# Optimization experiments

Measured on AMD Instinct MI355X. Metric: run time of the kernel, lower is better.

Reference implementation:

```python
import jax, jax.numpy as jnp
import numpy as np

TEMP = 0.07
W00 = 0.1
EPS = 1e-8


def setup_inputs() -> dict:
    key = jax.random.key(0)
    k1, k2, k3, k4 = jax.random.split(key, 4)
    B, N, D = 32, 256, 256
    M = B * N
    return {
        "audio_feats": jax.random.normal(k1, (B, N, D), dtype=jnp.float32),
        "visual_feats": jax.random.normal(k2, (B, N, D), dtype=jnp.float32),
        "audio_labels": jax.random.randint(k3, (M,), 0, 2, dtype=jnp.int64)
            if jax.config.jax_enable_x64 else jax.random.randint(k3, (M,), 0, 2, dtype=jnp.int32),
        "visual_labels": jax.random.randint(k4, (M,), 0, 2, dtype=jnp.int64)
            if jax.config.jax_enable_x64 else jax.random.randint(k4, (M,), 0, 2, dtype=jnp.int32),
    }


def reference(audio_feats, visual_feats, audio_labels, visual_labels):
    B, N, D = audio_feats.shape
    M = B * N
    a = audio_feats.reshape(M, D)
    v = visual_feats.reshape(M, D)
    # L2 normalize (torch F.normalize uses eps=1e-12 clamp on norm)
    a = a / jnp.maximum(jnp.linalg.norm(a, axis=-1, keepdims=True), 1e-12)
    v = v / jnp.maximum(jnp.linalg.norm(v, axis=-1, keepdims=True), 1e-12)
    sim = (a @ v.T) / TEMP  # (M, M)
    exp_sim = jnp.exp(sim)
    la = audio_labels[:, None]  # (M, 1)
    lv = visual_labels[None, :]  # (1, M)
    pos_mask = (la == lv) & ((la == 1) | (la == 0))
    weight = jnp.where(la == 1, 1.0, W00) * pos_mask.astype(sim.dtype)  # (M, M)
    wexp = exp_sim * weight

    # audio -> visual (row direction)
    denom_a2v = exp_sim.sum(axis=1)
    num_a2v = wexp.sum(axis=1)
    frac_a2v = (num_a2v + EPS) / (denom_a2v + EPS)
    valid_a2v = (num_a2v > 0).astype(sim.dtype)
    loss_a2v = -(valid_a2v * jnp.log(frac_a2v)).sum() / jnp.maximum(valid_a2v.sum(), 1.0)

    # visual -> audio (column direction)
    denom_v2a = exp_sim.sum(axis=0)
    num_v2a = wexp.sum(axis=0)
    frac_v2a = (num_v2a + EPS) / (denom_v2a + EPS)
    valid_v2a = (num_v2a > 0).astype(sim.dtype)
    loss_v2a = -(valid_v2a * jnp.log(frac_v2a)).sum() / jnp.maximum(valid_v2a.sum(), 1.0)

    return 0.5 * (loss_a2v + loss_v2a)
```

## Files before the change

### kernel.cpp

```cpp
#include <hip/hip_runtime.h>

#define M_ROWS 8192
#define D_DIM  256
#define BM     128
#define BN     128
#define NBI    (M_ROWS / BM)
#define NBJ    (M_ROWS / BN)
#define NJOBS  (NBI * NBJ)

#define ALPHA  4.53982478f


typedef __attribute__((ext_vector_type(4))) float  floatx4;

__device__ inline unsigned short f2bf(float f) {
    union { float f; unsigned int u; } v; v.f = f;
    unsigned int u = v.u;
    u = (u + 0x7fffu + ((u >> 16) & 1u)) >> 16;
    return (unsigned short)u;
}

__device__ inline float bf2f(unsigned short b) {
    union { unsigned int u; float f; } v; v.u = (unsigned int)b << 16;
    return v.f;
}

__device__ inline float fast_exp2(float x) {
#if __has_builtin(__builtin_amdgcn_exp2f)
    return __builtin_amdgcn_exp2f(x);
#else
    return exp2f(x);
#endif
}

__global__ __launch_bounds__(256) void normalize_kernel(
    const float* __restrict__ af, const float* __restrict__ vf,
    unsigned char* __restrict__ aB, unsigned char* __restrict__ vB,
    float* __restrict__ glob)
{
    __shared__ unsigned short tileS[16 * 264];

    if (blockIdx.x == 0) {
        if (threadIdx.x < 4) glob[threadIdx.x] = 0.f;
        if (threadIdx.x == 4) ((int*)glob)[4] = 0;
    }

    const int b = blockIdx.x;
    const bool isA = b < 512;
    const int T = isA ? b : b - 512;
    const float* src = (isA ? af : vf) + (size_t)T * 16 * D_DIM;
    unsigned char* dst = (isA ? aB : vB) + (size_t)T * 4096;

    const int t = threadIdx.x;
    const int row = t >> 4, c = t & 15;

    const float* p = src + row * D_DIM + c * 16;
    float4 x0 = ((const float4*)p)[0], x1 = ((const float4*)p)[1];
    float4 x2 = ((const float4*)p)[2], x3 = ((const float4*)p)[3];
    float ss = x0.x*x0.x + x0.y*x0.y + x0.z*x0.z + x0.w*x0.w
             + x1.x*x1.x + x1.y*x1.y + x1.z*x1.z + x1.w*x1.w
             + x2.x*x2.x + x2.y*x2.y + x2.z*x2.z + x2.w*x2.w
             + x3.x*x3.x + x3.y*x3.y + x3.z*x3.z + x3.w*x3.w;
    #pragma unroll
    for (int m = 1; m < 16; m <<= 1) ss += __shfl_xor(ss, m, 64);
    float scale = ALPHA / fmaxf(sqrtf(ss), 1e-12f);

    unsigned short* q = tileS + row * 264 + c * 16;
    ushort4 o0, o1, o2, o3;
    o0.x = f2bf(x0.x*scale); o0.y = f2bf(x0.y*scale); o0.z = f2bf(x0.z*scale); o0.w = f2bf(x0.w*scale);
    o1.x = f2bf(x1.x*scale); o1.y = f2bf(x1.y*scale); o1.z = f2bf(x1.z*scale); o1.w = f2bf(x1.w*scale);
    o2.x = f2bf(x2.x*scale); o2.y = f2bf(x2.y*scale); o2.z = f2bf(x2.z*scale); o2.w = f2bf(x2.w*scale);
    o3.x = f2bf(x3.x*scale); o3.y = f2bf(x3.y*scale); o3.z = f2bf(x3.z*scale); o3.w = f2bf(x3.w*scale);
    ((ushort4*)q)[0] = o0; ((ushort4*)q)[1] = o1;
    ((ushort4*)q)[2] = o2; ((ushort4*)q)[3] = o3;
    __syncthreads();

    #pragma unroll
    for (int s = 0; s < 2; ++s) {
        const int ch  = t + s * 256;
        const int l16 = ch & 15, quad = (ch >> 4) & 3, k32 = ch >> 6;
        const unsigned short* rp = &tileS[l16 * 264 + k32 * 32 + quad * 8];
        float f0 = bf2f(rp[0]), f1 = bf2f(rp[1]), f2 = bf2f(rp[2]), f3 = bf2f(rp[3]);
        float f4 = bf2f(rp[4]), f5 = bf2f(rp[5]), f6 = bf2f(rp[6]), f7 = bf2f(rp[7]);
        int p0 = __builtin_amdgcn_cvt_pk_fp8_f32(f0, f1, 0, false);
        p0     = __builtin_amdgcn_cvt_pk_fp8_f32(f2, f3, p0, true);
        int p1 = __builtin_amdgcn_cvt_pk_fp8_f32(f4, f5, 0, false);
        p1     = __builtin_amdgcn_cvt_pk_fp8_f32(f6, f7, p1, true);
        int2 outv; outv.x = p0; outv.y = p1;
        *(int2*)(dst + (size_t)ch * 8) = outv;
    }
}

__global__ __launch_bounds__(256, 3) void gemm_loss_kernel(
    const unsigned char* __restrict__ aB, const unsigned char* __restrict__ vB,
    const int* __restrict__ la, const int* __restrict__ lv,
    float* __restrict__ rowPart, float* __restrict__ colPart)
{
    const int tid  = threadIdx.x;
    const int wave = tid >> 6, lane = tid & 63;
    const int quad = lane >> 4, l16 = lane & 15;

    const int super = blockIdx.x >> 8;
    const int inner = blockIdx.x & 255;
    const int bx = (super & 3) * 16 + (inner & 15);
    const int by = (super >> 2) * 16 + (inner >> 4);
    const int i0 = bx * BM, j0 = by * BN;

    const unsigned char* Abase = aB + ((size_t)(bx * 8 + wave * 2) * 512 + lane) * 8;
    const unsigned char* Vbase = vB + ((size_t)(by * 8) * 512 + lane) * 8;

    floatx4 acc[2][8] = {};
    long long afr[3][2], bfr[3][8];

    #pragma unroll
    for (int s = 0; s < 2; ++s) {
        #pragma unroll
        for (int it = 0; it < 2; ++it)
            afr[s][it] = *(const long long*)(Abase + it * 4096 + s * 512);
        #pragma unroll
        for (int jt = 0; jt < 8; ++jt)
            bfr[s][jt] = *(const long long*)(Vbase + jt * 4096 + s * 512);
    }

    #pragma unroll
    for (int k32 = 0; k32 < 8; ++k32) {
        const int cur = k32 % 3;
        if (k32 < 6) {
            const int nx = (k32 + 2) % 3;
            const size_t ko = (size_t)(k32 + 2) * 512;
            #pragma unroll
            for (int it = 0; it < 2; ++it)
                afr[nx][it] = *(const long long*)(Abase + it * 4096 + ko);
            #pragma unroll
            for (int jt = 0; jt < 8; ++jt)
                bfr[nx][jt] = *(const long long*)(Vbase + jt * 4096 + ko);
        }
        #pragma unroll
        for (int it = 0; it < 2; ++it)
            #pragma unroll
            for (int jt = 0; jt < 8; ++jt)
                acc[it][jt] = __builtin_amdgcn_mfma_f32_16x16x32_fp8_fp8(
                    afr[cur][it], bfr[cur][jt], acc[it][jt], 0, 0, 0);
    }

    const int baseRow = i0 + wave * 32;
    float maf[2][4];
    #pragma unroll
    for (int it = 0; it < 2; ++it)
        #pragma unroll
        for (int r = 0; r < 4; ++r)
            maf[it][r] = (float)la[baseRow + it * 16 + quad * 4 + r];
    float mvf[8];
    #pragma unroll
    for (int jt = 0; jt < 8; ++jt)
        mvf[jt] = (float)lv[j0 + jt * 16 + l16];

    float rT[2][4] = {}, r1[2][4] = {};
    float cT[8] = {}, c1[8] = {};
    #pragma unroll
    for (int it = 0; it < 2; ++it) {
        #pragma unroll
        for (int jt = 0; jt < 8; ++jt) {
            #pragma unroll
            for (int r = 0; r < 4; ++r) {
                float e = fast_exp2(acc[it][jt][r]);
                rT[it][r] += e;
                r1[it][r] = fmaf(mvf[jt], e, r1[it][r]);
                cT[jt] += e;
                c1[jt] = fmaf(maf[it][r], e, c1[jt]);
            }
        }
    }

    #pragma unroll
    for (int jt = 0; jt < 8; ++jt) {
        float t0 = cT[jt], t1 = c1[jt];
        t0 += __shfl_xor(t0, 16, 64); t0 += __shfl_xor(t0, 32, 64);
        t1 += __shfl_xor(t1, 16, 64); t1 += __shfl_xor(t1, 32, 64);
        cT[jt] = t0; c1[jt] = t1;
    }

    __shared__ float rowbuf[2 * BM];
    __shared__ float colbuf[8 * BN];

    #pragma unroll
    for (int it = 0; it < 2; ++it) {
        #pragma unroll
        for (int r = 0; r < 4; ++r) {
            float s0 = rT[it][r], s1 = r1[it][r];
            #pragma unroll
            for (int m = 1; m < 16; m <<= 1) {
                s0 += __shfl_xor(s0, m, 64);
                s1 += __shfl_xor(s1, m, 64);
            }
            if (l16 == 0) {
                int rl = wave * 32 + it * 16 + quad * 4 + r;
                rowbuf[rl * 2 + 0] = s0;
                rowbuf[rl * 2 + 1] = s1;
            }
        }
    }
    if (quad == 0) {
        #pragma unroll
        for (int jt = 0; jt < 8; ++jt) {
            colbuf[(wave * 2 + 0) * BN + jt * 16 + l16] = cT[jt];
            colbuf[(wave * 2 + 1) * BN + jt * 16 + l16] = c1[jt];
        }
    }
    __syncthreads();

    {
        const int rl  = tid >> 1;
        const int cls = tid & 1;
        rowPart[((size_t)by * M_ROWS + i0 + rl) * 2 + cls] = rowbuf[rl * 2 + cls];
        float s = colbuf[(0 * 2 + cls) * BN + rl] + colbuf[(1 * 2 + cls) * BN + rl]
                + colbuf[(2 * 2 + cls) * BN + rl] + colbuf[(3 * 2 + cls) * BN + rl];
        colPart[((size_t)bx * M_ROWS + j0 + rl) * 2 + cls] = s;
    }
}

__global__ __launch_bounds__(256) void reduce_kernel(
    const float* __restrict__ rowPart, const float* __restrict__ colPart,
    const int* __restrict__ la, const int* __restrict__ lv,
    float* __restrict__ glob, float* __restrict__ out)
{
    const int bid = blockIdx.x;
    const bool aside = bid < 32;
    const int idx = (aside ? bid : bid - 32) * 256 + threadIdx.x;
    const float* part = aside ? rowPart : colPart;
    const int* lab = aside ? la : lv;

    float tot = 0.f, c1 = 0.f;
    #pragma unroll 4
    for (int b = 0; b < 64; ++b) {
        float2 p = *(const float2*)(part + ((size_t)b * M_ROWS + idx) * 2);
        tot += p.x; c1 += p.y;
    }
    float num = lab[idx] ? c1 : 0.1f * (tot - c1);
    float lg = 0.f, cnt = 0.f;
    if (num > 0.f) { lg = logf((num + 1e-8f) / (tot + 1e-8f)); cnt = 1.f; }

    #pragma unroll
    for (int m = 1; m < 64; m <<= 1) {
        lg  += __shfl_xor(lg,  m, 64);
        cnt += __shfl_xor(cnt, m, 64);
    }
    __shared__ float red[4][2];
    const int w = threadIdx.x >> 6, ln = threadIdx.x & 63;
    if (ln == 0) { red[w][0] = lg; red[w][1] = cnt; }
    __syncthreads();
    if (threadIdx.x == 0) {
        float slg  = red[0][0] + red[1][0] + red[2][0] + red[3][0];
        float scnt = red[0][1] + red[1][1] + red[2][1] + red[3][1];
        float* base = glob + (aside ? 0 : 2);
        atomicAdd(&base[0], slg);
        atomicAdd(&base[1], scnt);
        __threadfence();
        int old = atomicAdd((int*)glob + 4, 1);
        if (old == 63) {
            __threadfence();
            float sA = atomicAdd(&glob[0], 0.f);
            float cA = atomicAdd(&glob[1], 0.f);
            float sV = atomicAdd(&glob[2], 0.f);
            float cV = atomicAdd(&glob[3], 0.f);
            float lossA = -sA / fmaxf(cA, 1.f);
            float lossV = -sV / fmaxf(cV, 1.f);
            out[0] = 0.5f * (lossA + lossV);
        }
    }
}

extern "C" void kernel_launch(void* const* d_in, const int* in_sizes, int n_in,
                              void* d_out, int out_size, void* d_ws, size_t ws_size,
                              hipStream_t stream)
{
    const float* af = (const float*)d_in[0];
    const float* vf = (const float*)d_in[1];
    const int*   la = (const int*)d_in[2];
    const int*   lv = (const int*)d_in[3];
    float* out = (float*)d_out;

    char* ws = (char*)d_ws;
    unsigned char* aB = (unsigned char*)ws;
    unsigned char* vB = (unsigned char*)(ws + 2ull * 1024 * 1024);
    float* rowPart   = (float*)(ws +  4ull * 1024 * 1024);
    float* colPart   = (float*)(ws +  8ull * 1024 * 1024);
    float* glob      = (float*)(ws + 12ull * 1024 * 1024);

    normalize_kernel<<<1024, 256, 0, stream>>>(af, vf, aB, vB, glob);
    gemm_loss_kernel<<<NJOBS, 256, 0, stream>>>(aB, vB, la, lv, rowPart, colPart);
    reduce_kernel<<<64, 256, 0, stream>>>(rowPart, colPart, la, lv, glob, out);
}
```

Baseline: 131.0 us.

## Switch to 16x16x128 scaled FP8 MFMA with LDS-staged V tile and direct FP8 quantization

Replaces the 16x16x32 FP8 MFMA with the gfx950 scaled 16x16x128 f8f6f4 MFMA (unit scales), cutting the MFMA instruction count by four. The fp8 layout written by the normalize kernel is changed to match the wider operand fragments. Normalization now reduces the sum of squares through shared memory and quantizes straight to FP8, skipping the bf16 staging tile. In the GEMM kernel the whole 128x256 V tile is staged once in 32KB of LDS, and A fragments are loaded with 16-byte vector loads. The extra LDS footprint may reduce occupancy below the three blocks per CU the kernel requests.

```diff
diff --git a/kernel.cpp b/kernel.cpp
--- a/kernel.cpp
+++ b/kernel.cpp
@@ -11,19 +11,8 @@
 #define ALPHA  4.53982478f
 
 
-typedef __attribute__((ext_vector_type(4))) float  floatx4;
-
-__device__ inline unsigned short f2bf(float f) {
-    union { float f; unsigned int u; } v; v.f = f;
-    unsigned int u = v.u;
-    u = (u + 0x7fffu + ((u >> 16) & 1u)) >> 16;
-    return (unsigned short)u;
-}
-
-__device__ inline float bf2f(unsigned short b) {
-    union { unsigned int u; float f; } v; v.u = (unsigned int)b << 16;
-    return v.f;
-}
+typedef __attribute__((ext_vector_type(4))) float floatx4;
+typedef __attribute__((ext_vector_type(8))) int   intx8;
 
 __device__ inline float fast_exp2(float x) {
 #if __has_builtin(__builtin_amdgcn_exp2f)
@@ -33,12 +22,17 @@
 #endif
 }
 
+__device__ inline floatx4 mfma_fp8(intx8 a, intx8 b, floatx4 c) {
+    return __builtin_amdgcn_mfma_scale_f32_16x16x128_f8f6f4(
+        a, b, c, 0, 0, 0, 0x7f7f7f7f, 0, 0x7f7f7f7f);
+}
+
 __global__ __launch_bounds__(256) void normalize_kernel(
     const float* __restrict__ af, const float* __restrict__ vf,
     unsigned char* __restrict__ aB, unsigned char* __restrict__ vB,
     float* __restrict__ glob)
 {
-    __shared__ unsigned short tileS[16 * 264];
+    __shared__ float ssb[16][4];
 
     if (blockIdx.x == 0) {
         if (threadIdx.x < 4) glob[threadIdx.x] = 0.f;
@@ -51,44 +45,44 @@
     const float* src = (isA ? af : vf) + (size_t)T * 16 * D_DIM;
     unsigned char* dst = (isA ? aB : vB) + (size_t)T * 4096;
 
-    const int t = threadIdx.x;
-    const int row = t >> 4, c = t & 15;
-
-    const float* p = src + row * D_DIM + c * 16;
+    const int t    = threadIdx.x;
+    const int wave = t >> 6, lane = t & 63;
+    const int row  = t & 15;
+    const int kq   = (t >> 4) & 3;
+    const int h    = (t >> 6) & 1;
+    const int s    = t >> 7;
+    const int kbase = s * 128 + kq * 32 + h * 16;
+
+    const float* p = src + row * D_DIM + kbase;
     float4 x0 = ((const float4*)p)[0], x1 = ((const float4*)p)[1];
     float4 x2 = ((const float4*)p)[2], x3 = ((const float4*)p)[3];
+
     float ss = x0.x*x0.x + x0.y*x0.y + x0.z*x0.z + x0.w*x0.w
              + x1.x*x1.x + x1.y*x1.y + x1.z*x1.z + x1.w*x1.w
              + x2.x*x2.x + x2.y*x2.y + x2.z*x2.z + x2.w*x2.w
              + x3.x*x3.x + x3.y*x3.y + x3.z*x3.z + x3.w*x3.w;
-    #pragma unroll
-    for (int m = 1; m < 16; m <<= 1) ss += __shfl_xor(ss, m, 64);
-    float scale = ALPHA / fmaxf(sqrtf(ss), 1e-12f);
-
-    unsigned short* q = tileS + row * 264 + c * 16;
-    ushort4 o0, o1, o2, o3;
-    o0.x = f2bf(x0.x*scale); o0.y = f2bf(x0.y*scale); o0.z = f2bf(x0.z*scale); o0.w = f2bf(x0.w*scale);
-    o1.x = f2bf(x1.x*scale); o1.y = f2bf(x1.y*scale); o1.z = f2bf(x1.z*scale); o1.w = f2bf(x1.w*scale);
-    o2.x = f2bf(x2.x*scale); o2.y = f2bf(x2.y*scale); o2.z = f2bf(x2.z*scale); o2.w = f2bf(x2.w*scale);
-    o3.x = f2bf(x3.x*scale); o3.y = f2bf(x3.y*scale); o3.z = f2bf(x3.z*scale); o3.w = f2bf(x3.w*scale);
-    ((ushort4*)q)[0] = o0; ((ushort4*)q)[1] = o1;
-    ((ushort4*)q)[2] = o2; ((ushort4*)q)[3] = o3;
-    __syncthreads();
-
-    #pragma unroll
-    for (int s = 0; s < 2; ++s) {
-        const int ch  = t + s * 256;
-        const int l16 = ch & 15, quad = (ch >> 4) & 3, k32 = ch >> 6;
-        const unsigned short* rp = &tileS[l16 * 264 + k32 * 32 + quad * 8];
-        float f0 = bf2f(rp[0]), f1 = bf2f(rp[1]), f2 = bf2f(rp[2]), f3 = bf2f(rp[3]);
-        float f4 = bf2f(rp[4]), f5 = bf2f(rp[5]), f6 = bf2f(rp[6]), f7 = bf2f(rp[7]);
-        int p0 = __builtin_amdgcn_cvt_pk_fp8_f32(f0, f1, 0, false);
-        p0     = __builtin_amdgcn_cvt_pk_fp8_f32(f2, f3, p0, true);
-        int p1 = __builtin_amdgcn_cvt_pk_fp8_f32(f4, f5, 0, false);
-        p1     = __builtin_amdgcn_cvt_pk_fp8_f32(f6, f7, p1, true);
-        int2 outv; outv.x = p0; outv.y = p1;
-        *(int2*)(dst + (size_t)ch * 8) = outv;
-    }
+    ss += __shfl_xor(ss, 16, 64);
+    ss += __shfl_xor(ss, 32, 64);
+    if (lane < 16) ssb[lane][wave] = ss;
+    __syncthreads();
+    float tot = ssb[row][0] + ssb[row][1] + ssb[row][2] + ssb[row][3];
+    float scale = ALPHA / fmaxf(sqrtf(tot), 1e-12f);
+
+    int4 o;
+    int pk;
+    pk  = __builtin_amdgcn_cvt_pk_fp8_f32(x0.x*scale, x0.y*scale, 0, false);
+    pk  = __builtin_amdgcn_cvt_pk_fp8_f32(x0.z*scale, x0.w*scale, pk, true);
+    o.x = pk;
+    pk  = __builtin_amdgcn_cvt_pk_fp8_f32(x1.x*scale, x1.y*scale, 0, false);
+    pk  = __builtin_amdgcn_cvt_pk_fp8_f32(x1.z*scale, x1.w*scale, pk, true);
+    o.y = pk;
+    pk  = __builtin_amdgcn_cvt_pk_fp8_f32(x2.x*scale, x2.y*scale, 0, false);
+    pk  = __builtin_amdgcn_cvt_pk_fp8_f32(x2.z*scale, x2.w*scale, pk, true);
+    o.z = pk;
+    pk  = __builtin_amdgcn_cvt_pk_fp8_f32(x3.x*scale, x3.y*scale, 0, false);
+    pk  = __builtin_amdgcn_cvt_pk_fp8_f32(x3.z*scale, x3.w*scale, pk, true);
+    o.w = pk;
+    *(int4*)(dst + (size_t)t * 16) = o;
 }
 
 __global__ __launch_bounds__(256, 3) void gemm_loss_kernel(
@@ -96,6 +90,10 @@
     const int* __restrict__ la, const int* __restrict__ lv,
     float* __restrict__ rowPart, float* __restrict__ colPart)
 {
+    __shared__ unsigned char ldsB[32768];
+    __shared__ float rowbuf[2 * BM];
+    __shared__ float colbuf[8 * BN];
+
     const int tid  = threadIdx.x;
     const int wave = tid >> 6, lane = tid & 63;
     const int quad = lane >> 4, l16 = lane & 15;
@@ -106,41 +104,42 @@
     const int by = (super >> 2) * 16 + (inner >> 4);
     const int i0 = bx * BM, j0 = by * BN;
 
-    const unsigned char* Abase = aB + ((size_t)(bx * 8 + wave * 2) * 512 + lane) * 8;
-    const unsigned char* Vbase = vB + ((size_t)(by * 8) * 512 + lane) * 8;
+    {
+        const unsigned char* vsrc = vB + (size_t)by * 32768 + (size_t)wave * 8192
+                                       + (size_t)lane * 16;
+        unsigned char* ldst = ldsB + wave * 8192 + lane * 16;
+        #pragma unroll
+        for (int c = 0; c < 8; ++c)
+            *(int4*)(ldst + c * 1024) = *(const int4*)(vsrc + c * 1024);
+    }
+
+    const unsigned char* Abase = aB + (size_t)(bx * 8 + wave * 2) * 4096
+                                    + (size_t)lane * 16;
+    intx8 afr[2][2];
+    #pragma unroll
+    for (int it = 0; it < 2; ++it) {
+        #pragma unroll
+        for (int s = 0; s < 2; ++s) {
+            int4 h0 = *(const int4*)(Abase + it * 4096 + s * 2048);
+            int4 h1 = *(const int4*)(Abase + it * 4096 + s * 2048 + 1024);
+            afr[it][s] = intx8{h0.x, h0.y, h0.z, h0.w, h1.x, h1.y, h1.z, h1.w};
+        }
+    }
+
+    __syncthreads();
 
     floatx4 acc[2][8] = {};
-    long long afr[3][2], bfr[3][8];
-
+    const unsigned char* Bl = ldsB + lane * 16;
     #pragma unroll
     for (int s = 0; s < 2; ++s) {
         #pragma unroll
-        for (int it = 0; it < 2; ++it)
-            afr[s][it] = *(const long long*)(Abase + it * 4096 + s * 512);
-        #pragma unroll
-        for (int jt = 0; jt < 8; ++jt)
-            bfr[s][jt] = *(const long long*)(Vbase + jt * 4096 + s * 512);
-    }
-
-    #pragma unroll
-    for (int k32 = 0; k32 < 8; ++k32) {
-        const int cur = k32 % 3;
-        if (k32 < 6) {
-            const int nx = (k32 + 2) % 3;
-            const size_t ko = (size_t)(k32 + 2) * 512;
-            #pragma unroll
-            for (int it = 0; it < 2; ++it)
-                afr[nx][it] = *(const long long*)(Abase + it * 4096 + ko);
-            #pragma unroll
-            for (int jt = 0; jt < 8; ++jt)
-                bfr[nx][jt] = *(const long long*)(Vbase + jt * 4096 + ko);
-        }
-        #pragma unroll
-        for (int it = 0; it < 2; ++it)
-            #pragma unroll
-            for (int jt = 0; jt < 8; ++jt)
-                acc[it][jt] = __builtin_amdgcn_mfma_f32_16x16x32_fp8_fp8(
-                    afr[cur][it], bfr[cur][jt], acc[it][jt], 0, 0, 0);
+        for (int jt = 0; jt < 8; ++jt) {
+            int4 h0 = *(const int4*)(Bl + jt * 4096 + s * 2048);
+            int4 h1 = *(const int4*)(Bl + jt * 4096 + s * 2048 + 1024);
+            intx8 bf = intx8{h0.x, h0.y, h0.z, h0.w, h1.x, h1.y, h1.z, h1.w};
+            acc[0][jt] = mfma_fp8(afr[0][s], bf, acc[0][jt]);
+            acc[1][jt] = mfma_fp8(afr[1][s], bf, acc[1][jt]);
+        }
     }
 
     const int baseRow = i0 + wave * 32;
@@ -179,9 +178,6 @@
         t1 += __shfl_xor(t1, 16, 64); t1 += __shfl_xor(t1, 32, 64);
         cT[jt] = t0; c1[jt] = t1;
     }
-
-    __shared__ float rowbuf[2 * BM];
-    __shared__ float colbuf[8 * BN];
 
     #pragma unroll
     for (int it = 0; it < 2; ++it) {
```

After: 117.8 us. -10.1%, faster.
